# Performance work log

Hardware: AMD Instinct MI355X
Metric: run time of the kernel (lower is better)

The kernel has to match this reference:

```python
import jax, jax.numpy as jnp
import numpy as np

NUM_HEADS = 4
NUM_GROUPS = 8
EPS = 1e-5


def setup_inputs() -> dict:
    key = jax.random.key(0)
    ks = jax.random.split(key, 4)
    B, C, H, W = 4, 256, 64, 64
    x = jax.random.normal(ks[0], (B, C, H, W), dtype=jnp.float32)
    gn_w = jnp.ones((C,), dtype=jnp.float32)
    gn_b = jnp.zeros((C,), dtype=jnp.float32)
    # 1x1 convs == per-pixel matmuls; store kernels as [out_ch, in_ch]
    w_qkv = jax.random.normal(ks[1], (3 * C, C), dtype=jnp.float32) * (1.0 / np.sqrt(C))
    b_qkv = jnp.zeros((3 * C,), dtype=jnp.float32)
    w_proj = jax.random.normal(ks[2], (C, C), dtype=jnp.float32) * (1.0 / np.sqrt(C))
    b_proj = jnp.zeros((C,), dtype=jnp.float32)
    return {"x": x, "gn_w": gn_w, "gn_b": gn_b, "w_qkv": w_qkv,
            "b_qkv": b_qkv, "w_proj": w_proj, "b_proj": b_proj}


def reference(x, gn_w, gn_b, w_qkv, b_qkv, w_proj, b_proj):
    B, C, H, W = x.shape
    N = H * W
    nh = NUM_HEADS
    dh = C // nh

    # GroupNorm(8, C)
    xg = x.reshape(B, NUM_GROUPS, C // NUM_GROUPS, N)
    mu = jnp.mean(xg, axis=(2, 3), keepdims=True)
    var = jnp.var(xg, axis=(2, 3), keepdims=True)
    h = ((xg - mu) * jax.lax.rsqrt(var + EPS)).reshape(B, C, N)
    h = h * gn_w[None, :, None] + gn_b[None, :, None]

    # qkv 1x1 conv
    qkv = jnp.einsum('oc,bcn->bon', w_qkv, h) + b_qkv[None, :, None]
    q, k, v = jnp.split(qkv, 3, axis=1)  # each [B, C, N]
    q = q.reshape(B, nh, dh, N)
    k = k.reshape(B, nh, dh, N)
    v = v.reshape(B, nh, dh, N)

    # attn = softmax(q^T k / sqrt(dh)) over last dim -> [B, nh, N, N]
    scores = jnp.einsum('bhdi,bhdj->bhij', q, k) / jnp.sqrt(jnp.array(dh, dtype=x.dtype))
    attn = jax.nn.softmax(scores, axis=-1)

    # out = attn @ v^T, back to channel-major layout
    out = jnp.einsum('bhij,bhdj->bhdi', attn, v).reshape(B, C, N)

    # proj_out 1x1 conv + residual
    out = jnp.einsum('oc,bcn->bon', w_proj, out) + b_proj[None, :, None]
    return x + out.reshape(B, C, H, W)
```

## Files before the change

### kernel.cpp

```cpp
#include <hip/hip_runtime.h>
#include <math.h>

#define N_PIX 4096
#define C_CH  256
#define NH    4
#define DH    64

typedef __attribute__((ext_vector_type(8))) short bf16x8;
typedef __attribute__((ext_vector_type(4))) float f32x4;

static __device__ __forceinline__ unsigned short f2bf(float f) {
  union { float f; unsigned u; } v; v.f = f;
  unsigned r = v.u + 0x7fffu + ((v.u >> 16) & 1u);
  return (unsigned short)(r >> 16);
}
static __device__ __forceinline__ unsigned pk2(float a, float b) {
  return (unsigned)f2bf(a) | ((unsigned)f2bf(b) << 16);
}
static __device__ __forceinline__ unsigned pk2t(float a, float b) {
  return __builtin_amdgcn_perm(__float_as_uint(b), __float_as_uint(a),
                               0x07060302u);
}
#if __has_builtin(__builtin_amdgcn_exp2f)
#define EXP2(x) __builtin_amdgcn_exp2f(x)
#else
#define EXP2(x) exp2f(x)
#endif
static __device__ __forceinline__ int swz(int row, int g) {
  return (row << 6) + ((((row >> 2) ^ row ^ g) & 7) << 3);
}

__global__ __launch_bounds__(256) void gn_part_kernel(
    const float* __restrict__ x, const float* __restrict__ wqkv,
    const float* __restrict__ wproj, float* __restrict__ part,
    unsigned short* __restrict__ wB) {
  const int g = blockIdx.x, b = blockIdx.y, z = blockIdx.z;
  const int t = threadIdx.x;
  {
    const int bid = blockIdx.z * 32 + blockIdx.y * 8 + blockIdx.x;
    const int i = bid * 256 + t;
    const float* src = (i < 49152) ? (wqkv + (size_t)i * 4)
                                   : (wproj + (size_t)(i - 49152) * 4);
    float4 v = *(const float4*)src;
    uint2 u;
    u.x = pk2(v.x, v.y);
    u.y = pk2(v.z, v.w);
    *(uint2*)(wB + (size_t)i * 4) = u;
  }
  const float* base = x + (size_t)(b * C_CH + g * 32 + z * 4) * N_PIX;
  float sum = 0.f, sq = 0.f;
  for (int i = t * 4; i < 4 * N_PIX; i += 256 * 4) {
    float4 v = *(const float4*)(base + i);
    sum += v.x + v.y + v.z + v.w;
    sq  += v.x * v.x + v.y * v.y + v.z * v.z + v.w * v.w;
  }
  for (int off = 32; off >= 1; off >>= 1) {
    sum += __shfl_down(sum, off, 64);
    sq  += __shfl_down(sq,  off, 64);
  }
  __shared__ float ps[4], pq[4];
  if ((t & 63) == 0) { ps[t >> 6] = sum; pq[t >> 6] = sq; }
  __syncthreads();
  if (t == 0) {
    int idx = ((b * 8 + g) * 8 + z) * 2;
    part[idx + 0] = ps[0] + ps[1] + ps[2] + ps[3];
    part[idx + 1] = pq[0] + pq[1] + pq[2] + pq[3];
  }
}

__global__ __launch_bounds__(256) void gn_apply_kernel(
    const float* __restrict__ x, const float* __restrict__ part,
    const float* __restrict__ gn_w, const float* __restrict__ gn_b,
    unsigned short* __restrict__ hT) {
  const int n0 = blockIdx.x * 64;
  const int c0 = blockIdx.y * 64;
  const int b  = blockIdx.z;
  const int t  = threadIdx.x;
  __shared__ unsigned short Ht[64 * 64];
  __shared__ float ls[64], lsh[64];
  if (t < 64) {
    int c = c0 + t;
    int g = c >> 5;
    float S = 0.f, Q = 0.f;
#pragma unroll
    for (int z = 0; z < 8; ++z) {
      int idx = ((b * 8 + g) * 8 + z) * 2;
      S += part[idx + 0];
      Q += part[idx + 1];
    }
    const float inv_cnt = 1.f / (32.f * N_PIX);
    float mu  = S * inv_cnt;
    float var = Q * inv_cnt - mu * mu;
    float rstd = rsqrtf(var + 1e-5f);
    float s = rstd * gn_w[c];
    ls[t]  = s;
    lsh[t] = gn_b[c] - mu * s;
  }
  __syncthreads();
  const int cl = t >> 4;
  const int nl = (t & 15) * 4;
#pragma unroll
  for (int r = 0; r < 4; ++r) {
    int ce = cl + r * 16;
    float sv = ls[ce], sh = lsh[ce];
    float4 v =
        *(const float4*)(x + ((size_t)(b * C_CH + c0 + ce)) * N_PIX + n0 + nl);
#pragma unroll
    for (int i = 0; i < 4; ++i) {
      float f = ((const float*)&v)[i] * sv + sh;
      Ht[swz(nl + i, ce >> 3) + (ce & 7)] = f2bf(f);
    }
  }
  __syncthreads();
  {
    const int row = t >> 2, sg = (t & 3) * 2;
    uint4 o0 = *(const uint4*)&Ht[swz(row, sg + 0)];
    uint4 o1 = *(const uint4*)&Ht[swz(row, sg + 1)];
    size_t go = ((size_t)(b * N_PIX + n0 + row)) * C_CH + c0 + sg * 8;
    *(uint4*)(hT + go) = o0;
    *(uint4*)(hT + go + 8) = o1;
  }
}

__global__ __launch_bounds__(256) void qkv_gemm_kernel(
    const unsigned short* __restrict__ hT, const unsigned short* __restrict__ wB,
    const float* __restrict__ bqkv, unsigned short* __restrict__ qT,
    unsigned short* __restrict__ kT, unsigned short* __restrict__ vO) {
  const int mb = blockIdx.x, type = mb >> 2, head = mb & 3;
  const int n0 = blockIdx.y * 128;
  const int b  = blockIdx.z;
  const int t  = threadIdx.x;
  const int wave = t >> 6, lane = t & 63, quad = lane >> 4, lc = lane & 15;

  __shared__ unsigned short Ws[64 * 64];
  __shared__ unsigned short Hs[128 * 64];

  f32x4 acc[4][2];
#pragma unroll
  for (int i = 0; i < 4; ++i)
#pragma unroll
    for (int j = 0; j < 2; ++j) acc[i][j] = (f32x4){0.f, 0.f, 0.f, 0.f};

  const int wrow = t >> 2, wgb = (t & 3) * 2;
  const int hrow = t >> 1, hgb = (t & 1) * 4;
  const unsigned short* wp = wB + (size_t)(mb * 64 + wrow) * C_CH;
  const unsigned short* ap =
      hT + ((size_t)(b * N_PIX + n0 + hrow)) * C_CH + hgb * 8;

  for (int k0 = 0; k0 < C_CH; k0 += 64) {
    __syncthreads();
    {
      const unsigned short* s0 = wp + k0 + wgb * 8;
      uint4 u0 = *(const uint4*)(s0);
      uint4 u1 = *(const uint4*)(s0 + 8);
      *(uint4*)&Ws[swz(wrow, wgb + 0)] = u0;
      *(uint4*)&Ws[swz(wrow, wgb + 1)] = u1;
    }
    {
      const unsigned short* s0 = ap + k0;
#pragma unroll
      for (int j = 0; j < 4; ++j) {
        uint4 u = *(const uint4*)(s0 + j * 8);
        *(uint4*)&Hs[swz(hrow, hgb + j)] = u;
      }
    }
    __syncthreads();
#pragma unroll
    for (int kh = 0; kh < 2; ++kh) {
      bf16x8 wf[4], hf[2];
#pragma unroll
      for (int mt = 0; mt < 4; ++mt)
        wf[mt] = *(const bf16x8*)&Ws[swz(mt * 16 + lc, kh * 4 + quad)];
#pragma unroll
      for (int nt = 0; nt < 2; ++nt)
        hf[nt] = *(const bf16x8*)&Hs[swz(wave * 32 + nt * 16 + lc, kh * 4 + quad)];
      if (type < 2) {
#pragma unroll
        for (int mt = 0; mt < 4; ++mt)
#pragma unroll
          for (int nt = 0; nt < 2; ++nt)
            acc[mt][nt] = __builtin_amdgcn_mfma_f32_16x16x32_bf16(
                wf[mt], hf[nt], acc[mt][nt], 0, 0, 0);
      } else {
#pragma unroll
        for (int mt = 0; mt < 4; ++mt)
#pragma unroll
          for (int nt = 0; nt < 2; ++nt)
            acc[mt][nt] = __builtin_amdgcn_mfma_f32_16x16x32_bf16(
                hf[nt], wf[mt], acc[mt][nt], 0, 0, 0);
      }
    }
  }

  if (type < 2) {
    unsigned short* dst = (type == 0) ? qT : kT;
    const float qs = (type == 0) ? 0.125f * 1.44269504f : 1.0f;
#pragma unroll
    for (int mt = 0; mt < 4; ++mt)
#pragma unroll
      for (int nt = 0; nt < 2; ++nt) {
        int n = n0 + wave * 32 + nt * 16 + lc;
        int d0 = mt * 16 + quad * 4;
        float b0 = bqkv[mb * 64 + d0 + 0], b1 = bqkv[mb * 64 + d0 + 1];
        float b2 = bqkv[mb * 64 + d0 + 2], b3 = bqkv[mb * 64 + d0 + 3];
        uint2 w;
        w.x = pk2((acc[mt][nt][0] + b0) * qs, (acc[mt][nt][1] + b1) * qs);
        w.y = pk2((acc[mt][nt][2] + b2) * qs, (acc[mt][nt][3] + b3) * qs);
        *(uint2*)(dst + ((size_t)((b * NH + head) * N_PIX + n)) * 64 + d0) = w;
      }
  } else {
#pragma unroll
    for (int mt = 0; mt < 4; ++mt)
#pragma unroll
      for (int nt = 0; nt < 2; ++nt) {
        int d = mt * 16 + lc;
        float bias = bqkv[mb * 64 + d];
        int pix = n0 + wave * 32 + nt * 16 + quad * 4;
        uint2 w;
        w.x = pk2(acc[mt][nt][0] + bias, acc[mt][nt][1] + bias);
        w.y = pk2(acc[mt][nt][2] + bias, acc[mt][nt][3] + bias);
        *(uint2*)(vO + ((size_t)((b * NH + head) * 64 + d)) * N_PIX + pix) = w;
      }
  }
}

__global__ __launch_bounds__(256) void attn_kernel(
    const unsigned short* __restrict__ qT, const unsigned short* __restrict__ kT,
    const unsigned short* __restrict__ vO, unsigned short* __restrict__ aT) {
  const int t  = threadIdx.x;
  const int i0 = blockIdx.x * 128;
  const int h  = blockIdx.y;
  const int b  = blockIdx.z;
  const size_t bh = (size_t)(b * NH + h);
  const unsigned short* qp = qT + bh * N_PIX * 64;
  const unsigned short* kp = kT + bh * N_PIX * 64;
  const unsigned short* vp = vO + bh * 64 * N_PIX;

  __shared__ unsigned short Qt[128 * 64];
  __shared__ unsigned short Kt[64 * 64];
  __shared__ unsigned short Vs[64 * 64];
  unsigned short* const Ps = Qt;

  const int wave = t >> 6, lane = t & 63, quad = lane >> 4, lc = lane & 15;
  const int qb0 = wave * 32, qb1 = wave * 32 + 16;
  const int srow = t >> 2, sg = (t & 3) * 2;
  const int qrow = t >> 1, qg = (t & 1) * 4;

  {
    const unsigned short* s = qp + (size_t)(i0 + qrow) * 64 + qg * 8;
#pragma unroll
    for (int i = 0; i < 4; ++i) {
      uint4 u = *(const uint4*)(s + i * 8);
      *(uint4*)&Qt[swz(qrow, qg + i)] = u;
    }
  }
  __syncthreads();
  bf16x8 aq[2][2];
  aq[0][0] = *(const bf16x8*)&Qt[swz(qb0 + lc, quad)];
  aq[0][1] = *(const bf16x8*)&Qt[swz(qb0 + lc, quad + 4)];
  aq[1][0] = *(const bf16x8*)&Qt[swz(qb1 + lc, quad)];
  aq[1][1] = *(const bf16x8*)&Qt[swz(qb1 + lc, quad + 4)];

  int kof0[4], kof1[4], vof0[4], vof1[4], pw[2][4];
#pragma unroll
  for (int jt = 0; jt < 4; ++jt) {
    kof0[jt] = swz(jt * 16 + lc, quad);
    kof1[jt] = swz(jt * 16 + lc, quad + 4);
    pw[0][jt] = swz(qb0 + lc, jt * 2 + (quad >> 1)) + (quad & 1) * 4;
    pw[1][jt] = swz(qb1 + lc, jt * 2 + (quad >> 1)) + (quad & 1) * 4;
  }
#pragma unroll
  for (int mt = 0; mt < 4; ++mt) {
    vof0[mt] = swz(mt * 16 + lc, quad);
    vof1[mt] = swz(mt * 16 + lc, quad + 4);
  }
  const int pb00 = swz(qb0 + lc, quad), pb01 = swz(qb0 + lc, quad + 4);
  const int pb10 = swz(qb1 + lc, quad), pb11 = swz(qb1 + lc, quad + 4);
  const bf16x8 ones = {16256, 16256, 16256, 16256, 16256, 16256, 16256, 16256};

  f32x4 la0 = (f32x4){0.f, 0.f, 0.f, 0.f};
  f32x4 la1 = (f32x4){0.f, 0.f, 0.f, 0.f};
  f32x4 od[2][4];
#pragma unroll
  for (int qh = 0; qh < 2; ++qh)
#pragma unroll
    for (int mt = 0; mt < 4; ++mt) od[qh][mt] = (f32x4){0.f, 0.f, 0.f, 0.f};

  for (int j0 = 0; j0 < N_PIX; j0 += 64) {
    __syncthreads();
    {
      const unsigned short* sk = kp + (size_t)(j0 + srow) * 64 + sg * 8;
      uint4 k0 = *(const uint4*)(sk);
      uint4 k1 = *(const uint4*)(sk + 8);
      *(uint4*)&Kt[swz(srow, sg + 0)] = k0;
      *(uint4*)&Kt[swz(srow, sg + 1)] = k1;
      const unsigned short* sv = vp + (size_t)srow * N_PIX + j0 + sg * 8;
      uint4 v0 = *(const uint4*)(sv);
      uint4 v1 = *(const uint4*)(sv + 8);
      *(uint4*)&Vs[swz(srow, sg + 0)] = v0;
      *(uint4*)&Vs[swz(srow, sg + 1)] = v1;
    }
    __syncthreads();

#pragma unroll
    for (int jt = 0; jt < 4; ++jt) {
      bf16x8 bk0 = *(const bf16x8*)&Kt[kof0[jt]];
      bf16x8 bk1 = *(const bf16x8*)&Kt[kof1[jt]];
      f32x4 a0 = (f32x4){0.f, 0.f, 0.f, 0.f};
      a0 = __builtin_amdgcn_mfma_f32_16x16x32_bf16(bk0, aq[0][0], a0, 0, 0, 0);
      a0 = __builtin_amdgcn_mfma_f32_16x16x32_bf16(bk1, aq[0][1], a0, 0, 0, 0);
      f32x4 a1 = (f32x4){0.f, 0.f, 0.f, 0.f};
      a1 = __builtin_amdgcn_mfma_f32_16x16x32_bf16(bk0, aq[1][0], a1, 0, 0, 0);
      a1 = __builtin_amdgcn_mfma_f32_16x16x32_bf16(bk1, aq[1][1], a1, 0, 0, 0);
      uint2 u0, u1;
      u0.x = pk2t(EXP2(a0[0]), EXP2(a0[1]));
      u0.y = pk2t(EXP2(a0[2]), EXP2(a0[3]));
      u1.x = pk2t(EXP2(a1[0]), EXP2(a1[1]));
      u1.y = pk2t(EXP2(a1[2]), EXP2(a1[3]));
      *(uint2*)&Ps[pw[0][jt]] = u0;
      *(uint2*)&Ps[pw[1][jt]] = u1;
    }

    bf16x8 bp00 = *(const bf16x8*)&Ps[pb00];
    bf16x8 bp01 = *(const bf16x8*)&Ps[pb01];
    bf16x8 bp10 = *(const bf16x8*)&Ps[pb10];
    bf16x8 bp11 = *(const bf16x8*)&Ps[pb11];
    la0 = __builtin_amdgcn_mfma_f32_16x16x32_bf16(ones, bp00, la0, 0, 0, 0);
    la0 = __builtin_amdgcn_mfma_f32_16x16x32_bf16(ones, bp01, la0, 0, 0, 0);
    la1 = __builtin_amdgcn_mfma_f32_16x16x32_bf16(ones, bp10, la1, 0, 0, 0);
    la1 = __builtin_amdgcn_mfma_f32_16x16x32_bf16(ones, bp11, la1, 0, 0, 0);

#pragma unroll
    for (int mt = 0; mt < 4; ++mt) {
      bf16x8 av0 = *(const bf16x8*)&Vs[vof0[mt]];
      bf16x8 av1 = *(const bf16x8*)&Vs[vof1[mt]];
      od[0][mt] =
          __builtin_amdgcn_mfma_f32_16x16x32_bf16(av0, bp00, od[0][mt], 0, 0, 0);
      od[0][mt] =
          __builtin_amdgcn_mfma_f32_16x16x32_bf16(av1, bp01, od[0][mt], 0, 0, 0);
      od[1][mt] =
          __builtin_amdgcn_mfma_f32_16x16x32_bf16(av0, bp10, od[1][mt], 0, 0, 0);
      od[1][mt] =
          __builtin_amdgcn_mfma_f32_16x16x32_bf16(av1, bp11, od[1][mt], 0, 0, 0);
    }
  }

  float inv0 = 1.f / la0[0];
  float inv1 = 1.f / la1[0];
#pragma unroll
  for (int mt = 0; mt < 4; ++mt) {
    uint2 u0, u1;
    u0.x = pk2(od[0][mt][0] * inv0, od[0][mt][1] * inv0);
    u0.y = pk2(od[0][mt][2] * inv0, od[0][mt][3] * inv0);
    u1.x = pk2(od[1][mt][0] * inv1, od[1][mt][1] * inv1);
    u1.y = pk2(od[1][mt][2] * inv1, od[1][mt][3] * inv1);
    *(uint2*)&Ps[swz(qb0 + lc, mt * 2 + (quad >> 1)) + (quad & 1) * 4] = u0;
    *(uint2*)&Ps[swz(qb1 + lc, mt * 2 + (quad >> 1)) + (quad & 1) * 4] = u1;
  }
  __syncthreads();
  {
    size_t go = ((size_t)(b * N_PIX + i0 + qrow)) * C_CH + h * 64 + qg * 8;
#pragma unroll
    for (int i = 0; i < 4; ++i) {
      uint4 o = *(const uint4*)&Ps[swz(qrow, qg + i)];
      *(uint4*)(aT + go + i * 8) = o;
    }
  }
}

__global__ __launch_bounds__(256) void proj_gemm_kernel(
    const unsigned short* __restrict__ aT, const unsigned short* __restrict__ wPB,
    const float* __restrict__ bproj, const float* __restrict__ x,
    float* __restrict__ out) {
  const int m0 = blockIdx.x * 64;
  const int n0 = blockIdx.y * 128;
  const int b  = blockIdx.z;
  const int t  = threadIdx.x;
  const int wave = t >> 6, lane = t & 63, quad = lane >> 4, lc = lane & 15;

  __shared__ unsigned short Ws[64 * 64];
  __shared__ unsigned short Hs[128 * 64];

  f32x4 acc[4][2];
#pragma unroll
  for (int i = 0; i < 4; ++i)
#pragma unroll
    for (int j = 0; j < 2; ++j) acc[i][j] = (f32x4){0.f, 0.f, 0.f, 0.f};

  const int wrow = t >> 2, wgb = (t & 3) * 2;
  const int hrow = t >> 1, hgb = (t & 1) * 4;
  const unsigned short* wp = wPB + (size_t)(m0 + wrow) * C_CH;
  const unsigned short* ap =
      aT + ((size_t)(b * N_PIX + n0 + hrow)) * C_CH + hgb * 8;

  for (int k0 = 0; k0 < C_CH; k0 += 64) {
    __syncthreads();
    {
      const unsigned short* s0 = wp + k0 + wgb * 8;
      uint4 u0 = *(const uint4*)(s0);
      uint4 u1 = *(const uint4*)(s0 + 8);
      *(uint4*)&Ws[swz(wrow, wgb + 0)] = u0;
      *(uint4*)&Ws[swz(wrow, wgb + 1)] = u1;
    }
    {
      const unsigned short* s0 = ap + k0;
#pragma unroll
      for (int j = 0; j < 4; ++j) {
        uint4 u = *(const uint4*)(s0 + j * 8);
        *(uint4*)&Hs[swz(hrow, hgb + j)] = u;
      }
    }
    __syncthreads();
#pragma unroll
    for (int kh = 0; kh < 2; ++kh) {
      bf16x8 wf[4], hf[2];
#pragma unroll
      for (int mt = 0; mt < 4; ++mt)
        wf[mt] = *(const bf16x8*)&Ws[swz(mt * 16 + lc, kh * 4 + quad)];
#pragma unroll
      for (int nt = 0; nt < 2; ++nt)
        hf[nt] = *(const bf16x8*)&Hs[swz(wave * 32 + nt * 16 + lc, kh * 4 + quad)];
#pragma unroll
      for (int mt = 0; mt < 4; ++mt)
#pragma unroll
        for (int nt = 0; nt < 2; ++nt)
          acc[mt][nt] = __builtin_amdgcn_mfma_f32_16x16x32_bf16(
              wf[mt], hf[nt], acc[mt][nt], 0, 0, 0);
    }
  }
#pragma unroll
  for (int mt = 0; mt < 4; ++mt) {
#pragma unroll
    for (int nt = 0; nt < 2; ++nt) {
      int n = n0 + wave * 32 + nt * 16 + lc;
#pragma unroll
      for (int r = 0; r < 4; ++r) {
        int c = m0 + mt * 16 + quad * 4 + r;
        size_t gi = ((size_t)(b * C_CH + c)) * N_PIX + n;
        out[gi] = acc[mt][nt][r] + bproj[c] + x[gi];
      }
    }
  }
}

extern "C" void kernel_launch(void* const* d_in, const int* in_sizes, int n_in,
                              void* d_out, int out_size, void* d_ws,
                              size_t ws_size, hipStream_t stream) {
  const float* x      = (const float*)d_in[0];
  const float* gn_w   = (const float*)d_in[1];
  const float* gn_b   = (const float*)d_in[2];
  const float* w_qkv  = (const float*)d_in[3];
  const float* b_qkv  = (const float*)d_in[4];
  const float* w_proj = (const float*)d_in[5];
  const float* b_proj = (const float*)d_in[6];
  float* out = (float*)d_out;

  float* ws   = (float*)d_ws;
  float* part = ws + 2048;
  unsigned short* qT = (unsigned short*)(ws + 4096);
  unsigned short* kT = qT + (size_t)4194304;
  unsigned short* vO = kT + (size_t)4194304;
  unsigned short* aT = vO + (size_t)4194304;
  unsigned short* hT = aT + (size_t)4194304;
  unsigned short* wB = hT + (size_t)4 * N_PIX * C_CH;
  unsigned short* wPB = wB + (size_t)49152 * 4;

  gn_part_kernel<<<dim3(8, 4, 8), dim3(256), 0, stream>>>(x, w_qkv, w_proj,
                                                          part, wB);
  gn_apply_kernel<<<dim3(64, 4, 4), dim3(256), 0, stream>>>(x, part, gn_w,
                                                            gn_b, hT);
  qkv_gemm_kernel<<<dim3(12, 32, 4), dim3(256), 0, stream>>>(
      hT, wB, b_qkv, qT, kT, vO);
  attn_kernel<<<dim3(32, 4, 4), dim3(256), 0, stream>>>(qT, kT, vO, aT);
  proj_gemm_kernel<<<dim3(4, 32, 4), dim3(256), 0, stream>>>(
      aT, wPB, b_proj, x, out);
}
```

Baseline: 223.2 us.

## Double-buffer LDS tiles with register prefetch in GEMM and attention kernels

Converts the QKV GEMM, attention and projection GEMM main loops to a double-buffered shared-memory scheme. The next K/V or weight/activation tile is loaded into registers before the MFMA work on the current buffer, then written to the other buffer, which leaves one barrier per iteration instead of two. The aim is to hide global load latency behind compute. In exchange, shared memory per block doubles and register pressure rises, which may reduce occupancy. The last iteration issues one redundant wrap-around prefetch.

After: 233.2 us. 1.04x slower.

```diff
diff --git a/kernel.cpp b/kernel.cpp
--- a/kernel.cpp
+++ b/kernel.cpp
@@ -132,8 +132,8 @@
   const int t  = threadIdx.x;
   const int wave = t >> 6, lane = t & 63, quad = lane >> 4, lc = lane & 15;
 
-  __shared__ unsigned short Ws[64 * 64];
-  __shared__ unsigned short Hs[128 * 64];
+  __shared__ unsigned short Ws[2 * 64 * 64];
+  __shared__ unsigned short Hs[2 * 128 * 64];
 
   f32x4 acc[4][2];
 #pragma unroll
@@ -143,37 +143,46 @@
 
   const int wrow = t >> 2, wgb = (t & 3) * 2;
   const int hrow = t >> 1, hgb = (t & 1) * 4;
-  const unsigned short* wp = wB + (size_t)(mb * 64 + wrow) * C_CH;
+  const unsigned short* wp = wB + (size_t)(mb * 64 + wrow) * C_CH + wgb * 8;
   const unsigned short* ap =
       hT + ((size_t)(b * N_PIX + n0 + hrow)) * C_CH + hgb * 8;
-
-  for (int k0 = 0; k0 < C_CH; k0 += 64) {
-    __syncthreads();
-    {
-      const unsigned short* s0 = wp + k0 + wgb * 8;
-      uint4 u0 = *(const uint4*)(s0);
-      uint4 u1 = *(const uint4*)(s0 + 8);
-      *(uint4*)&Ws[swz(wrow, wgb + 0)] = u0;
-      *(uint4*)&Ws[swz(wrow, wgb + 1)] = u1;
-    }
-    {
-      const unsigned short* s0 = ap + k0;
-#pragma unroll
-      for (int j = 0; j < 4; ++j) {
-        uint4 u = *(const uint4*)(s0 + j * 8);
-        *(uint4*)&Hs[swz(hrow, hgb + j)] = u;
-      }
-    }
-    __syncthreads();
+  const int wsw0 = swz(wrow, wgb + 0), wsw1 = swz(wrow, wgb + 1);
+  int hsw[4];
+#pragma unroll
+  for (int j = 0; j < 4; ++j) hsw[j] = swz(hrow, hgb + j);
+
+  {
+    uint4 w0 = *(const uint4*)(wp);
+    uint4 w1 = *(const uint4*)(wp + 8);
+    *(uint4*)&Ws[wsw0] = w0;
+    *(uint4*)&Ws[wsw1] = w1;
+#pragma unroll
+    for (int j = 0; j < 4; ++j) {
+      uint4 u = *(const uint4*)(ap + j * 8);
+      *(uint4*)&Hs[hsw[j]] = u;
+    }
+  }
+  __syncthreads();
+
+  for (int kc = 0; kc < 4; ++kc) {
+    const int cw = (kc & 1) * 4096, ch = (kc & 1) * 8192;
+    const int nw = 4096 - cw, nh = 8192 - ch;
+    const int kn = ((kc + 1) & 3) * 64;
+    uint4 pw0 = *(const uint4*)(wp + kn);
+    uint4 pw1 = *(const uint4*)(wp + kn + 8);
+    uint4 ph[4];
+#pragma unroll
+    for (int j = 0; j < 4; ++j) ph[j] = *(const uint4*)(ap + kn + j * 8);
 #pragma unroll
     for (int kh = 0; kh < 2; ++kh) {
       bf16x8 wf[4], hf[2];
 #pragma unroll
       for (int mt = 0; mt < 4; ++mt)
-        wf[mt] = *(const bf16x8*)&Ws[swz(mt * 16 + lc, kh * 4 + quad)];
+        wf[mt] = *(const bf16x8*)&Ws[cw + swz(mt * 16 + lc, kh * 4 + quad)];
 #pragma unroll
       for (int nt = 0; nt < 2; ++nt)
-        hf[nt] = *(const bf16x8*)&Hs[swz(wave * 32 + nt * 16 + lc, kh * 4 + quad)];
+        hf[nt] =
+            *(const bf16x8*)&Hs[ch + swz(wave * 32 + nt * 16 + lc, kh * 4 + quad)];
       if (type < 2) {
 #pragma unroll
         for (int mt = 0; mt < 4; ++mt)
@@ -190,6 +199,11 @@
                 hf[nt], wf[mt], acc[mt][nt], 0, 0, 0);
       }
     }
+    *(uint4*)&Ws[nw + wsw0] = pw0;
+    *(uint4*)&Ws[nw + wsw1] = pw1;
+#pragma unroll
+    for (int j = 0; j < 4; ++j) *(uint4*)&Hs[nh + hsw[j]] = ph[j];
+    __syncthreads();
   }
 
   if (type < 2) {
@@ -237,8 +251,8 @@
   const unsigned short* vp = vO + bh * 64 * N_PIX;
 
   __shared__ unsigned short Qt[128 * 64];
-  __shared__ unsigned short Kt[64 * 64];
-  __shared__ unsigned short Vs[64 * 64];
+  __shared__ unsigned short Kt[2 * 64 * 64];
+  __shared__ unsigned short Vs[2 * 64 * 64];
   unsigned short* const Ps = Qt;
 
   const int wave = t >> 6, lane = t & 63, quad = lane >> 4, lc = lane & 15;
@@ -277,6 +291,21 @@
   const int pb00 = swz(qb0 + lc, quad), pb01 = swz(qb0 + lc, quad + 4);
   const int pb10 = swz(qb1 + lc, quad), pb11 = swz(qb1 + lc, quad + 4);
   const bf16x8 ones = {16256, 16256, 16256, 16256, 16256, 16256, 16256, 16256};
+  const int wsw0 = swz(srow, sg + 0), wsw1 = swz(srow, sg + 1);
+
+  {
+    const unsigned short* sk = kp + (size_t)srow * 64 + sg * 8;
+    const unsigned short* sv = vp + (size_t)srow * N_PIX + sg * 8;
+    uint4 k0 = *(const uint4*)(sk);
+    uint4 k1 = *(const uint4*)(sk + 8);
+    uint4 v0 = *(const uint4*)(sv);
+    uint4 v1 = *(const uint4*)(sv + 8);
+    *(uint4*)&Kt[wsw0] = k0;
+    *(uint4*)&Kt[wsw1] = k1;
+    *(uint4*)&Vs[wsw0] = v0;
+    *(uint4*)&Vs[wsw1] = v1;
+  }
+  __syncthreads();
 
   f32x4 la0 = (f32x4){0.f, 0.f, 0.f, 0.f};
   f32x4 la1 = (f32x4){0.f, 0.f, 0.f, 0.f};
@@ -286,26 +315,22 @@
 #pragma unroll
     for (int mt = 0; mt < 4; ++mt) od[qh][mt] = (f32x4){0.f, 0.f, 0.f, 0.f};
 
-  for (int j0 = 0; j0 < N_PIX; j0 += 64) {
-    __syncthreads();
-    {
-      const unsigned short* sk = kp + (size_t)(j0 + srow) * 64 + sg * 8;
-      uint4 k0 = *(const uint4*)(sk);
-      uint4 k1 = *(const uint4*)(sk + 8);
-      *(uint4*)&Kt[swz(srow, sg + 0)] = k0;
-      *(uint4*)&Kt[swz(srow, sg + 1)] = k1;
-      const unsigned short* sv = vp + (size_t)srow * N_PIX + j0 + sg * 8;
-      uint4 v0 = *(const uint4*)(sv);
-      uint4 v1 = *(const uint4*)(sv + 8);
-      *(uint4*)&Vs[swz(srow, sg + 0)] = v0;
-      *(uint4*)&Vs[swz(srow, sg + 1)] = v1;
-    }
-    __syncthreads();
+  for (int it = 0; it < 64; ++it) {
+    const int cb = (it & 1) << 12;
+    const int nb = 4096 - cb;
+    const int jn = ((it + 1) & 63) * 64;
+
+    const unsigned short* snk = kp + (size_t)(jn + srow) * 64 + sg * 8;
+    const unsigned short* snv = vp + (size_t)srow * N_PIX + jn + sg * 8;
+    uint4 pk0 = *(const uint4*)(snk);
+    uint4 pk1 = *(const uint4*)(snk + 8);
+    uint4 pv0 = *(const uint4*)(snv);
+    uint4 pv1 = *(const uint4*)(snv + 8);
 
 #pragma unroll
     for (int jt = 0; jt < 4; ++jt) {
-      bf16x8 bk0 = *(const bf16x8*)&Kt[kof0[jt]];
-      bf16x8 bk1 = *(const bf16x8*)&Kt[kof1[jt]];
+      bf16x8 bk0 = *(const bf16x8*)&Kt[cb + kof0[jt]];
+      bf16x8 bk1 = *(const bf16x8*)&Kt[cb + kof1[jt]];
       f32x4 a0 = (f32x4){0.f, 0.f, 0.f, 0.f};
       a0 = __builtin_amdgcn_mfma_f32_16x16x32_bf16(bk0, aq[0][0], a0, 0, 0, 0);
       a0 = __builtin_amdgcn_mfma_f32_16x16x32_bf16(bk1, aq[0][1], a0, 0, 0, 0);
@@ -329,11 +354,10 @@
     la0 = __builtin_amdgcn_mfma_f32_16x16x32_bf16(ones, bp01, la0, 0, 0, 0);
     la1 = __builtin_amdgcn_mfma_f32_16x16x32_bf16(ones, bp10, la1, 0, 0, 0);
     la1 = __builtin_amdgcn_mfma_f32_16x16x32_bf16(ones, bp11, la1, 0, 0, 0);
-
 #pragma unroll
     for (int mt = 0; mt < 4; ++mt) {
-      bf16x8 av0 = *(const bf16x8*)&Vs[vof0[mt]];
-      bf16x8 av1 = *(const bf16x8*)&Vs[vof1[mt]];
+      bf16x8 av0 = *(const bf16x8*)&Vs[cb + vof0[mt]];
+      bf16x8 av1 = *(const bf16x8*)&Vs[cb + vof1[mt]];
       od[0][mt] =
           __builtin_amdgcn_mfma_f32_16x16x32_bf16(av0, bp00, od[0][mt], 0, 0, 0);
       od[0][mt] =
@@ -343,6 +367,12 @@
       od[1][mt] =
           __builtin_amdgcn_mfma_f32_16x16x32_bf16(av1, bp11, od[1][mt], 0, 0, 0);
     }
+
+    *(uint4*)&Kt[nb + wsw0] = pk0;
+    *(uint4*)&Kt[nb + wsw1] = pk1;
+    *(uint4*)&Vs[nb + wsw0] = pv0;
+    *(uint4*)&Vs[nb + wsw1] = pv1;
+    __syncthreads();
   }
 
   float inv0 = 1.f / la0[0];
@@ -378,8 +408,8 @@
   const int t  = threadIdx.x;
   const int wave = t >> 6, lane = t & 63, quad = lane >> 4, lc = lane & 15;
 
-  __shared__ unsigned short Ws[64 * 64];
-  __shared__ unsigned short Hs[128 * 64];
+  __shared__ unsigned short Ws[2 * 64 * 64];
+  __shared__ unsigned short Hs[2 * 128 * 64];
 
   f32x4 acc[4][2];
 #pragma unroll
@@ -389,37 +419,46 @@
 
   const int wrow = t >> 2, wgb = (t & 3) * 2;
   const int hrow = t >> 1, hgb = (t & 1) * 4;
-  const unsigned short* wp = wPB + (size_t)(m0 + wrow) * C_CH;
+  const unsigned short* wp = wPB + (size_t)(m0 + wrow) * C_CH + wgb * 8;
   const unsigned short* ap =
       aT + ((size_t)(b * N_PIX + n0 + hrow)) * C_CH + hgb * 8;
-
-  for (int k0 = 0; k0 < C_CH; k0 += 64) {
-    __syncthreads();
-    {
-      const unsigned short* s0 = wp + k0 + wgb * 8;
-      uint4 u0 = *(const uint4*)(s0);
-      uint4 u1 = *(const uint4*)(s0 + 8);
-      *(uint4*)&Ws[swz(wrow, wgb + 0)] = u0;
-      *(uint4*)&Ws[swz(wrow, wgb + 1)] = u1;
-    }
-    {
-      const unsigned short* s0 = ap + k0;
-#pragma unroll
-      for (int j = 0; j < 4; ++j) {
-        uint4 u = *(const uint4*)(s0 + j * 8);
-        *(uint4*)&Hs[swz(hrow, hgb + j)] = u;
-      }
-    }
-    __syncthreads();
+  const int wsw0 = swz(wrow, wgb + 0), wsw1 = swz(wrow, wgb + 1);
+  int hsw[4];
+#pragma unroll
+  for (int j = 0; j < 4; ++j) hsw[j] = swz(hrow, hgb + j);
+
+  {
+    uint4 w0 = *(const uint4*)(wp);
+    uint4 w1 = *(const uint4*)(wp + 8);
+    *(uint4*)&Ws[wsw0] = w0;
+    *(uint4*)&Ws[wsw1] = w1;
+#pragma unroll
+    for (int j = 0; j < 4; ++j) {
+      uint4 u = *(const uint4*)(ap + j * 8);
+      *(uint4*)&Hs[hsw[j]] = u;
+    }
+  }
+  __syncthreads();
+
+  for (int kc = 0; kc < 4; ++kc) {
+    const int cw = (kc & 1) * 4096, ch = (kc & 1) * 8192;
+    const int nw = 4096 - cw, nh = 8192 - ch;
+    const int kn = ((kc + 1) & 3) * 64;
+    uint4 pw0 = *(const uint4*)(wp + kn);
+    uint4 pw1 = *(const uint4*)(wp + kn + 8);
+    uint4 ph[4];
+#pragma unroll
+    for (int j = 0; j < 4; ++j) ph[j] = *(const uint4*)(ap + kn + j * 8);
 #pragma unroll
     for (int kh = 0; kh < 2; ++kh) {
       bf16x8 wf[4], hf[2];
 #pragma unroll
       for (int mt = 0; mt < 4; ++mt)
-        wf[mt] = *(const bf16x8*)&Ws[swz(mt * 16 + lc, kh * 4 + quad)];
+        wf[mt] = *(const bf16x8*)&Ws[cw + swz(mt * 16 + lc, kh * 4 + quad)];
 #pragma unroll
       for (int nt = 0; nt < 2; ++nt)
-        hf[nt] = *(const bf16x8*)&Hs[swz(wave * 32 + nt * 16 + lc, kh * 4 + quad)];
+        hf[nt] =
+            *(const bf16x8*)&Hs[ch + swz(wave * 32 + nt * 16 + lc, kh * 4 + quad)];
 #pragma unroll
       for (int mt = 0; mt < 4; ++mt)
 #pragma unroll
@@ -427,6 +466,11 @@
           acc[mt][nt] = __builtin_amdgcn_mfma_f32_16x16x32_bf16(
               wf[mt], hf[nt], acc[mt][nt], 0, 0, 0);
     }
+    *(uint4*)&Ws[nw + wsw0] = pw0;
+    *(uint4*)&Ws[nw + wsw1] = pw1;
+#pragma unroll
+    for (int j = 0; j < 4; ++j) *(uint4*)&Hs[nh + hsw[j]] = ph[j];
+    __syncthreads();
   }
 #pragma unroll
   for (int mt = 0; mt < 4; ++mt) {
```

## Split attention over two key halves and merge partials in a combine kernel

Applied to the files above, without the earlier changes.

The attention kernel now splits the key/value range into two halves, launching twice as many blocks (512 instead of 256). Each half writes unnormalized bf16 partial outputs and row sums, and a new combine kernel adds them and normalizes. This is split-K for flash attention, aimed at better occupancy across the many CUs, since 256 blocks underfill the GPU. It costs an extra kernel launch, extra global traffic for the partials, and some bf16 rounding of the unnormalized partials. No max subtraction is done, so the partials can be summed directly.

Measured after the change: 232.9 us. +4.3%, slower.

```diff
diff --git a/kernel.cpp b/kernel.cpp
--- a/kernel.cpp
+++ b/kernel.cpp
@@ -20,6 +20,12 @@
 static __device__ __forceinline__ unsigned pk2t(float a, float b) {
   return __builtin_amdgcn_perm(__float_as_uint(b), __float_as_uint(a),
                                0x07060302u);
+}
+static __device__ __forceinline__ float bflo(unsigned u) {
+  return __uint_as_float(u << 16);
+}
+static __device__ __forceinline__ float bfhi(unsigned u) {
+  return __uint_as_float(u & 0xffff0000u);
 }
 #if __has_builtin(__builtin_amdgcn_exp2f)
 #define EXP2(x) __builtin_amdgcn_exp2f(x)
@@ -226,15 +232,18 @@
 
 __global__ __launch_bounds__(256) void attn_kernel(
     const unsigned short* __restrict__ qT, const unsigned short* __restrict__ kT,
-    const unsigned short* __restrict__ vO, unsigned short* __restrict__ aT) {
+    const unsigned short* __restrict__ vO, unsigned short* __restrict__ oP,
+    float* __restrict__ lP) {
   const int t  = threadIdx.x;
   const int i0 = blockIdx.x * 128;
   const int h  = blockIdx.y;
-  const int b  = blockIdx.z;
-  const size_t bh = (size_t)(b * NH + h);
-  const unsigned short* qp = qT + bh * N_PIX * 64;
-  const unsigned short* kp = kT + bh * N_PIX * 64;
-  const unsigned short* vp = vO + bh * 64 * N_PIX;
+  const int b  = blockIdx.z >> 1;
+  const int s  = blockIdx.z & 1;
+  const int bh = b * NH + h;
+  const size_t bhs = (size_t)bh;
+  const unsigned short* qp = qT + bhs * N_PIX * 64;
+  const unsigned short* kp = kT + bhs * N_PIX * 64;
+  const unsigned short* vp = vO + bhs * 64 * N_PIX;
 
   __shared__ unsigned short Qt[128 * 64];
   __shared__ unsigned short Kt[64 * 64];
@@ -247,10 +256,10 @@
   const int qrow = t >> 1, qg = (t & 1) * 4;
 
   {
-    const unsigned short* s = qp + (size_t)(i0 + qrow) * 64 + qg * 8;
+    const unsigned short* sp = qp + (size_t)(i0 + qrow) * 64 + qg * 8;
 #pragma unroll
     for (int i = 0; i < 4; ++i) {
-      uint4 u = *(const uint4*)(s + i * 8);
+      uint4 u = *(const uint4*)(sp + i * 8);
       *(uint4*)&Qt[swz(qrow, qg + i)] = u;
     }
   }
@@ -286,7 +295,9 @@
 #pragma unroll
     for (int mt = 0; mt < 4; ++mt) od[qh][mt] = (f32x4){0.f, 0.f, 0.f, 0.f};
 
-  for (int j0 = 0; j0 < N_PIX; j0 += 64) {
+  const int jbase = s * 2048;
+  for (int it = 0; it < 32; ++it) {
+    const int j0 = jbase + it * 64;
     __syncthreads();
     {
       const unsigned short* sk = kp + (size_t)(j0 + srow) * 64 + sg * 8;
@@ -329,7 +340,6 @@
     la0 = __builtin_amdgcn_mfma_f32_16x16x32_bf16(ones, bp01, la0, 0, 0, 0);
     la1 = __builtin_amdgcn_mfma_f32_16x16x32_bf16(ones, bp10, la1, 0, 0, 0);
     la1 = __builtin_amdgcn_mfma_f32_16x16x32_bf16(ones, bp11, la1, 0, 0, 0);
-
 #pragma unroll
     for (int mt = 0; mt < 4; ++mt) {
       bf16x8 av0 = *(const bf16x8*)&Vs[vof0[mt]];
@@ -345,27 +355,52 @@
     }
   }
 
-  float inv0 = 1.f / la0[0];
-  float inv1 = 1.f / la1[0];
+  if (quad == 0) {
+    float* lrow = lP + ((size_t)(s * 16 + bh)) * N_PIX + i0;
+    lrow[qb0 + lc] = la0[0];
+    lrow[qb1 + lc] = la1[0];
+  }
+
 #pragma unroll
   for (int mt = 0; mt < 4; ++mt) {
     uint2 u0, u1;
-    u0.x = pk2(od[0][mt][0] * inv0, od[0][mt][1] * inv0);
-    u0.y = pk2(od[0][mt][2] * inv0, od[0][mt][3] * inv0);
-    u1.x = pk2(od[1][mt][0] * inv1, od[1][mt][1] * inv1);
-    u1.y = pk2(od[1][mt][2] * inv1, od[1][mt][3] * inv1);
+    u0.x = pk2(od[0][mt][0], od[0][mt][1]);
+    u0.y = pk2(od[0][mt][2], od[0][mt][3]);
+    u1.x = pk2(od[1][mt][0], od[1][mt][1]);
+    u1.y = pk2(od[1][mt][2], od[1][mt][3]);
     *(uint2*)&Ps[swz(qb0 + lc, mt * 2 + (quad >> 1)) + (quad & 1) * 4] = u0;
     *(uint2*)&Ps[swz(qb1 + lc, mt * 2 + (quad >> 1)) + (quad & 1) * 4] = u1;
   }
   __syncthreads();
   {
+    unsigned short* dst = oP + (size_t)s * 4194304;
     size_t go = ((size_t)(b * N_PIX + i0 + qrow)) * C_CH + h * 64 + qg * 8;
 #pragma unroll
     for (int i = 0; i < 4; ++i) {
       uint4 o = *(const uint4*)&Ps[swz(qrow, qg + i)];
-      *(uint4*)(aT + go + i * 8) = o;
-    }
-  }
+      *(uint4*)(dst + go + i * 8) = o;
+    }
+  }
+}
+
+__global__ __launch_bounds__(256) void combine_kernel(
+    const unsigned short* __restrict__ oP, const float* __restrict__ lP,
+    unsigned short* __restrict__ aT) {
+  const size_t idx = ((size_t)blockIdx.x * 256 + threadIdx.x) * 8;
+  const int c = (int)(idx & 255);
+  const int n = (int)((idx >> 8) & 4095);
+  const int b = (int)(idx >> 20);
+  const int bh = b * NH + (c >> 6);
+  float l = lP[(size_t)bh * N_PIX + n] + lP[(size_t)(16 + bh) * N_PIX + n];
+  float inv = 1.f / l;
+  uint4 u1 = *(const uint4*)(oP + idx);
+  uint4 u2 = *(const uint4*)(oP + 4194304 + idx);
+  uint4 r;
+  r.x = pk2((bflo(u1.x) + bflo(u2.x)) * inv, (bfhi(u1.x) + bfhi(u2.x)) * inv);
+  r.y = pk2((bflo(u1.y) + bflo(u2.y)) * inv, (bfhi(u1.y) + bfhi(u2.y)) * inv);
+  r.z = pk2((bflo(u1.z) + bflo(u2.z)) * inv, (bfhi(u1.z) + bfhi(u2.z)) * inv);
+  r.w = pk2((bflo(u1.w) + bflo(u2.w)) * inv, (bfhi(u1.w) + bfhi(u2.w)) * inv);
+  *(uint4*)(aT + idx) = r;
 }
 
 __global__ __launch_bounds__(256) void proj_gemm_kernel(
@@ -462,8 +497,10 @@
   unsigned short* vO = kT + (size_t)4194304;
   unsigned short* aT = vO + (size_t)4194304;
   unsigned short* hT = aT + (size_t)4194304;
-  unsigned short* wB = hT + (size_t)4 * N_PIX * C_CH;
+  unsigned short* wB = hT + (size_t)4194304;
   unsigned short* wPB = wB + (size_t)49152 * 4;
+  unsigned short* oP = wB + (size_t)262144;
+  float* lP = (float*)(oP + (size_t)8388608);
 
   gn_part_kernel<<<dim3(8, 4, 8), dim3(256), 0, stream>>>(x, w_qkv, w_proj,
                                                           part, wB);
@@ -471,7 +508,8 @@
                                                             gn_b, hT);
   qkv_gemm_kernel<<<dim3(12, 32, 4), dim3(256), 0, stream>>>(
       hT, wB, b_qkv, qT, kT, vO);
-  attn_kernel<<<dim3(32, 4, 4), dim3(256), 0, stream>>>(qT, kT, vO, aT);
+  attn_kernel<<<dim3(32, 4, 8), dim3(256), 0, stream>>>(qT, kT, vO, oP, lP);
+  combine_kernel<<<dim3(2048), dim3(256), 0, stream>>>(oP, lP, aT);
   proj_gemm_kernel<<<dim3(4, 32, 4), dim3(256), 0, stream>>>(
       aT, wPB, b_proj, x, out);
 }
```

## Double-buffer K/V tiles and software-pipeline QK^T with PV in attention

Applied to the files above, without the earlier changes.

The attention kernel now keeps two K/V tile buffers in LDS and register-prefetches the next tile from global memory while computing on the current one. The loop is skewed so that the QK^T MFMAs for tile it overlap with the PV MFMAs and exp2 for tile it-1. The row-sum is also moved from ones-vector MFMAs to scalar adds with a final cross-lane shuffle reduction. This aims to hide global load latency and remove MFMA work spent on the softmax denominator, at the cost of more LDS and registers, which may lower occupancy.

Result: faster. 214.9 us (-3.7%).

```diff
diff --git a/kernel.cpp b/kernel.cpp
--- a/kernel.cpp
+++ b/kernel.cpp
@@ -237,8 +237,8 @@
   const unsigned short* vp = vO + bh * 64 * N_PIX;
 
   __shared__ unsigned short Qt[128 * 64];
-  __shared__ unsigned short Kt[64 * 64];
-  __shared__ unsigned short Vs[64 * 64];
+  __shared__ unsigned short Kt[2 * 64 * 64];
+  __shared__ unsigned short Vs[2 * 64 * 64];
   unsigned short* const Ps = Qt;
 
   const int wave = t >> 6, lane = t & 63, quad = lane >> 4, lc = lane & 15;
@@ -247,10 +247,10 @@
   const int qrow = t >> 1, qg = (t & 1) * 4;
 
   {
-    const unsigned short* s = qp + (size_t)(i0 + qrow) * 64 + qg * 8;
+    const unsigned short* sp = qp + (size_t)(i0 + qrow) * 64 + qg * 8;
 #pragma unroll
     for (int i = 0; i < 4; ++i) {
-      uint4 u = *(const uint4*)(s + i * 8);
+      uint4 u = *(const uint4*)(sp + i * 8);
       *(uint4*)&Qt[swz(qrow, qg + i)] = u;
     }
   }
@@ -276,32 +276,34 @@
   }
   const int pb00 = swz(qb0 + lc, quad), pb01 = swz(qb0 + lc, quad + 4);
   const int pb10 = swz(qb1 + lc, quad), pb11 = swz(qb1 + lc, quad + 4);
-  const bf16x8 ones = {16256, 16256, 16256, 16256, 16256, 16256, 16256, 16256};
-
-  f32x4 la0 = (f32x4){0.f, 0.f, 0.f, 0.f};
-  f32x4 la1 = (f32x4){0.f, 0.f, 0.f, 0.f};
+  const int sw0 = swz(srow, sg + 0), sw1 = swz(srow, sg + 1);
+  const unsigned short* kbase = kp + (size_t)srow * 64 + sg * 8;
+  const unsigned short* vbase = vp + (size_t)srow * N_PIX + sg * 8;
+
+  float la0 = 0.f, la1 = 0.f;
   f32x4 od[2][4];
 #pragma unroll
   for (int qh = 0; qh < 2; ++qh)
 #pragma unroll
     for (int mt = 0; mt < 4; ++mt) od[qh][mt] = (f32x4){0.f, 0.f, 0.f, 0.f};
 
-  for (int j0 = 0; j0 < N_PIX; j0 += 64) {
-    __syncthreads();
-    {
-      const unsigned short* sk = kp + (size_t)(j0 + srow) * 64 + sg * 8;
-      uint4 k0 = *(const uint4*)(sk);
-      uint4 k1 = *(const uint4*)(sk + 8);
-      *(uint4*)&Kt[swz(srow, sg + 0)] = k0;
-      *(uint4*)&Kt[swz(srow, sg + 1)] = k1;
-      const unsigned short* sv = vp + (size_t)srow * N_PIX + j0 + sg * 8;
-      uint4 v0 = *(const uint4*)(sv);
-      uint4 v1 = *(const uint4*)(sv + 8);
-      *(uint4*)&Vs[swz(srow, sg + 0)] = v0;
-      *(uint4*)&Vs[swz(srow, sg + 1)] = v1;
-    }
-    __syncthreads();
-
+  {
+    uint4 k0 = *(const uint4*)(kbase);
+    uint4 k1 = *(const uint4*)(kbase + 8);
+    uint4 v0 = *(const uint4*)(vbase);
+    uint4 v1 = *(const uint4*)(vbase + 8);
+    *(uint4*)&Kt[sw0] = k0;
+    *(uint4*)&Kt[sw1] = k1;
+    *(uint4*)&Vs[sw0] = v0;
+    *(uint4*)&Vs[sw1] = v1;
+  }
+  __syncthreads();
+
+  {
+    uint4 pk0 = *(const uint4*)(kbase + 4096);
+    uint4 pk1 = *(const uint4*)(kbase + 4096 + 8);
+    uint4 pv0 = *(const uint4*)(vbase + 64);
+    uint4 pv1 = *(const uint4*)(vbase + 64 + 8);
 #pragma unroll
     for (int jt = 0; jt < 4; ++jt) {
       bf16x8 bk0 = *(const bf16x8*)&Kt[kof0[jt]];
@@ -312,28 +314,62 @@
       f32x4 a1 = (f32x4){0.f, 0.f, 0.f, 0.f};
       a1 = __builtin_amdgcn_mfma_f32_16x16x32_bf16(bk0, aq[1][0], a1, 0, 0, 0);
       a1 = __builtin_amdgcn_mfma_f32_16x16x32_bf16(bk1, aq[1][1], a1, 0, 0, 0);
-      uint2 u0, u1;
-      u0.x = pk2t(EXP2(a0[0]), EXP2(a0[1]));
-      u0.y = pk2t(EXP2(a0[2]), EXP2(a0[3]));
-      u1.x = pk2t(EXP2(a1[0]), EXP2(a1[1]));
-      u1.y = pk2t(EXP2(a1[2]), EXP2(a1[3]));
+      float e0 = EXP2(a0[0]), e1 = EXP2(a0[1]), e2 = EXP2(a0[2]),
+            e3 = EXP2(a0[3]);
+      la0 += (e0 + e1) + (e2 + e3);
+      uint2 u0;
+      u0.x = pk2t(e0, e1);
+      u0.y = pk2t(e2, e3);
       *(uint2*)&Ps[pw[0][jt]] = u0;
+      float f0 = EXP2(a1[0]), f1 = EXP2(a1[1]), f2 = EXP2(a1[2]),
+            f3 = EXP2(a1[3]);
+      la1 += (f0 + f1) + (f2 + f3);
+      uint2 u1;
+      u1.x = pk2t(f0, f1);
+      u1.y = pk2t(f2, f3);
       *(uint2*)&Ps[pw[1][jt]] = u1;
+    }
+    *(uint4*)&Kt[4096 + sw0] = pk0;
+    *(uint4*)&Kt[4096 + sw1] = pk1;
+    *(uint4*)&Vs[4096 + sw0] = pv0;
+    *(uint4*)&Vs[4096 + sw1] = pv1;
+  }
+
+  for (int it = 1; it < 64; ++it) {
+    const int cb = (it & 1) << 12;
+    const int ob = 4096 - cb;
+    __syncthreads();
+    const size_t kadv = (size_t)((it + 1) & 63) * 4096;
+    const size_t vadv = (size_t)((it + 1) & 63) * 64;
+    uint4 pk0 = *(const uint4*)(kbase + kadv);
+    uint4 pk1 = *(const uint4*)(kbase + kadv + 8);
+    uint4 pv0 = *(const uint4*)(vbase + vadv);
+    uint4 pv1 = *(const uint4*)(vbase + vadv + 8);
+
+    f32x4 s0[4], s1[4];
+#pragma unroll
+    for (int jt = 0; jt < 4; ++jt) {
+      bf16x8 bk0 = *(const bf16x8*)&Kt[cb + kof0[jt]];
+      bf16x8 bk1 = *(const bf16x8*)&Kt[cb + kof1[jt]];
+      f32x4 a0 = (f32x4){0.f, 0.f, 0.f, 0.f};
+      a0 = __builtin_amdgcn_mfma_f32_16x16x32_bf16(bk0, aq[0][0], a0, 0, 0, 0);
+      a0 = __builtin_amdgcn_mfma_f32_16x16x32_bf16(bk1, aq[0][1], a0, 0, 0, 0);
+      f32x4 a1 = (f32x4){0.f, 0.f, 0.f, 0.f};
+      a1 = __builtin_amdgcn_mfma_f32_16x16x32_bf16(bk0, aq[1][0], a1, 0, 0, 0);
+      a1 = __builtin_amdgcn_mfma_f32_16x16x32_bf16(bk1, aq[1][1], a1, 0, 0, 0);
+      s0[jt] = a0;
+      s1[jt] = a1;
     }
 
     bf16x8 bp00 = *(const bf16x8*)&Ps[pb00];
     bf16x8 bp01 = *(const bf16x8*)&Ps[pb01];
     bf16x8 bp10 = *(const bf16x8*)&Ps[pb10];
     bf16x8 bp11 = *(const bf16x8*)&Ps[pb11];
-    la0 = __builtin_amdgcn_mfma_f32_16x16x32_bf16(ones, bp00, la0, 0, 0, 0);
-    la0 = __builtin_amdgcn_mfma_f32_16x16x32_bf16(ones, bp01, la0, 0, 0, 0);
-    la1 = __builtin_amdgcn_mfma_f32_16x16x32_bf16(ones, bp10, la1, 0, 0, 0);
-    la1 = __builtin_amdgcn_mfma_f32_16x16x32_bf16(ones, bp11, la1, 0, 0, 0);
 
 #pragma unroll
     for (int mt = 0; mt < 4; ++mt) {
-      bf16x8 av0 = *(const bf16x8*)&Vs[vof0[mt]];
-      bf16x8 av1 = *(const bf16x8*)&Vs[vof1[mt]];
+      bf16x8 av0 = *(const bf16x8*)&Vs[ob + vof0[mt]];
+      bf16x8 av1 = *(const bf16x8*)&Vs[ob + vof1[mt]];
       od[0][mt] =
           __builtin_amdgcn_mfma_f32_16x16x32_bf16(av0, bp00, od[0][mt], 0, 0, 0);
       od[0][mt] =
@@ -342,11 +378,56 @@
           __builtin_amdgcn_mfma_f32_16x16x32_bf16(av0, bp10, od[1][mt], 0, 0, 0);
       od[1][mt] =
           __builtin_amdgcn_mfma_f32_16x16x32_bf16(av1, bp11, od[1][mt], 0, 0, 0);
-    }
-  }
-
-  float inv0 = 1.f / la0[0];
-  float inv1 = 1.f / la1[0];
+      float e0 = EXP2(s0[mt][0]), e1 = EXP2(s0[mt][1]), e2 = EXP2(s0[mt][2]),
+            e3 = EXP2(s0[mt][3]);
+      la0 += (e0 + e1) + (e2 + e3);
+      uint2 u0;
+      u0.x = pk2t(e0, e1);
+      u0.y = pk2t(e2, e3);
+      *(uint2*)&Ps[pw[0][mt]] = u0;
+      float f0 = EXP2(s1[mt][0]), f1 = EXP2(s1[mt][1]), f2 = EXP2(s1[mt][2]),
+            f3 = EXP2(s1[mt][3]);
+      la1 += (f0 + f1) + (f2 + f3);
+      uint2 u1;
+      u1.x = pk2t(f0, f1);
+      u1.y = pk2t(f2, f3);
+      *(uint2*)&Ps[pw[1][mt]] = u1;
+    }
+
+    __syncthreads();
+    *(uint4*)&Kt[ob + sw0] = pk0;
+    *(uint4*)&Kt[ob + sw1] = pk1;
+    *(uint4*)&Vs[ob + sw0] = pv0;
+    *(uint4*)&Vs[ob + sw1] = pv1;
+  }
+
+  {
+    bf16x8 bp00 = *(const bf16x8*)&Ps[pb00];
+    bf16x8 bp01 = *(const bf16x8*)&Ps[pb01];
+    bf16x8 bp10 = *(const bf16x8*)&Ps[pb10];
+    bf16x8 bp11 = *(const bf16x8*)&Ps[pb11];
+#pragma unroll
+    for (int mt = 0; mt < 4; ++mt) {
+      bf16x8 av0 = *(const bf16x8*)&Vs[4096 + vof0[mt]];
+      bf16x8 av1 = *(const bf16x8*)&Vs[4096 + vof1[mt]];
+      od[0][mt] =
+          __builtin_amdgcn_mfma_f32_16x16x32_bf16(av0, bp00, od[0][mt], 0, 0, 0);
+      od[0][mt] =
+          __builtin_amdgcn_mfma_f32_16x16x32_bf16(av1, bp01, od[0][mt], 0, 0, 0);
+      od[1][mt] =
+          __builtin_amdgcn_mfma_f32_16x16x32_bf16(av0, bp10, od[1][mt], 0, 0, 0);
+      od[1][mt] =
+          __builtin_amdgcn_mfma_f32_16x16x32_bf16(av1, bp11, od[1][mt], 0, 0, 0);
+    }
+  }
+
+  la0 += __shfl_xor(la0, 16, 64);
+  la0 += __shfl_xor(la0, 32, 64);
+  la1 += __shfl_xor(la1, 16, 64);
+  la1 += __shfl_xor(la1, 32, 64);
+  float inv0 = 1.f / la0;
+  float inv1 = 1.f / la1;
+
 #pragma unroll
   for (int mt = 0; mt < 4; ++mt) {
     uint2 u0, u1;
@@ -462,7 +543,7 @@
   unsigned short* vO = kT + (size_t)4194304;
   unsigned short* aT = vO + (size_t)4194304;
   unsigned short* hT = aT + (size_t)4194304;
-  unsigned short* wB = hT + (size_t)4 * N_PIX * C_CH;
+  unsigned short* wB = hT + (size_t)4194304;
   unsigned short* wPB = wB + (size_t)49152 * 4;
 
   gn_part_kernel<<<dim3(8, 4, 8), dim3(256), 0, stream>>>(x, w_qkv, w_proj,
```
